# Optimization experiments

Measured on AMD Instinct MI355X. Metric: run time of the kernel, lower is better.

The kernel has to match this reference:

```python
import jax, jax.numpy as jnp
import numpy as np

B, L, NE, DOUT = 4, 4096, 64, 64
DI = 128          # backbone model dim (hardcoded d_inner in MambaDoc)
NL = 2            # num_layers
H = 2             # num_heads
N = 128           # state_dim
G = 1             # num_groups
CONV = 4          # conv_size
DIN = 2 * DI      # expand=2 -> 256 inner channels of the mixer
P = DIN // H      # headdim = 128
CCH = DIN + 2 * G * N      # 512 conv channels (x, B, C)
DPROJ = 2 * DIN + 2 * G * N + H  # 770 in_proj output width


def setup_inputs() -> dict:
    key = jax.random.key(0)
    ks = jax.random.split(key, 8)
    s = lambda k, shape, sc: (jax.random.normal(k, shape, jnp.float32) * sc)
    return {
        "x": s(ks[0], (B, L, NE), 1.0),
        "in_w": s(ks[1], (DI, NE), (1.0 / NE) ** 0.5),
        "in_b": jnp.zeros((DI,), jnp.float32),
        "out_w": s(ks[2], (DOUT, DI), (1.0 / DI) ** 0.5),
        "out_b": jnp.zeros((DOUT,), jnp.float32),
        "l_rms_w": jnp.ones((NL, DI), jnp.float32),
        "l_in_w": s(ks[3], (NL, DPROJ, DI), (1.0 / DI) ** 0.5),
        "conv_w": s(ks[4], (NL, CCH, CONV), (1.0 / CONV) ** 0.5),
        "conv_b": jnp.zeros((NL, CCH), jnp.float32),
        "dt_bias": s(ks[5], (NL, H), 0.1),
        "A_log": jnp.zeros((NL, H), jnp.float32),   # A = -exp(A_log) = -1
        "D_p": jnp.ones((NL, H), jnp.float32),
        "gnorm_w": jnp.ones((NL, DIN), jnp.float32),
        "l_out_w": s(ks[6], (NL, DI, DIN), (1.0 / DIN) ** 0.5),
        "fnorm_w": jnp.ones((DI,), jnp.float32),
    }


def _rms(x, w, eps=1e-5):
    return x * jax.lax.rsqrt(jnp.mean(x * x, -1, keepdims=True) + eps) * w


def _mamba_layer(x, rms_w, in_w, cw, cb, dtb, a_log, d, gnw, ow):
    # x: (B,L,DI)
    h = _rms(x, rms_w)
    zxbcdt = jnp.einsum("bld,ed->ble", h, in_w)  # (B,L,770)
    z, xBC, dt = jnp.split(zxbcdt, [DIN, DIN + CCH], axis=-1)
    # causal depthwise conv over time, conv_size taps
    xp = jnp.pad(xBC, ((0, 0), (CONV - 1, 0), (0, 0)))
    xc = cb + sum(xp[:, k:k + L, :] * cw[:, k] for k in range(CONV))
    xc = jax.nn.silu(xc)
    xs, Bm, Cm = jnp.split(xc, [DIN, DIN + G * N], axis=-1)
    xs = xs.reshape(B, L, H, P)
    dt = jax.nn.softplus(dt + dtb)                 # (B,L,H)
    dA = jnp.exp(dt * (-jnp.exp(a_log)))           # (B,L,H) discrete decay

    def step(hc, inp):
        dA_t, dt_t, x_t, B_t, C_t = inp  # (B,H),(B,H),(B,H,P),(B,N),(B,N)
        hc = hc * dA_t[:, :, None, None] + (dt_t[:, :, None] * x_t)[..., None] * B_t[:, None, None, :]
        y = jnp.einsum("bhpn,bn->bhp", hc, C_t)
        return hc, y

    h0 = jnp.zeros((B, H, P, N), x.dtype)
    seq = (jnp.moveaxis(dA, 1, 0), jnp.moveaxis(dt, 1, 0), jnp.moveaxis(xs, 1, 0),
           jnp.moveaxis(Bm, 1, 0), jnp.moveaxis(Cm, 1, 0))
    _, ys = jax.lax.scan(step, h0, seq)
    y = jnp.moveaxis(ys, 0, 1)                     # (B,L,H,P)
    y = y + xs * d[None, None, :, None]            # D skip connection
    y = _rms(y.reshape(B, L, DIN) * jax.nn.silu(z), gnw)  # gated RMSNorm
    return x + jnp.einsum("ble,de->bld", y, ow)


def reference(x, in_w, in_b, out_w, out_b, l_rms_w, l_in_w, conv_w, conv_b,
              dt_bias, A_log, D_p, gnorm_w, l_out_w, fnorm_w):
    xp = jnp.einsum("bln,dn->bld", x, in_w) + in_b
    h = xp
    for i in range(NL):
        h = _mamba_layer(h, l_rms_w[i], l_in_w[i], conv_w[i], conv_b[i],
                         dt_bias[i], A_log[i], D_p[i], gnorm_w[i], l_out_w[i])
    h = _rms(h, fnorm_w)            # backbone final norm
    out = xp + h                    # outer residual in MambaDoc.forward
    return jnp.einsum("bld,od->blo", out, out_w) + out_b
```

## Files before the change

kernel.cpp:

```cpp
#include <hip/hip_runtime.h>
#include <cstddef>
#include <cstdint>


#define LSEQ 4096
#define MTOK 16384

typedef unsigned short u16;
typedef _Float16 f16x8 __attribute__((ext_vector_type(8)));
typedef float f32x4 __attribute__((ext_vector_type(4)));

__device__ __forceinline__ u16 f2h(float x) {
    return __builtin_bit_cast(u16, (_Float16)x);
}
__device__ __forceinline__ float h2f(u16 u) {
    return (float)__builtin_bit_cast(_Float16, u);
}
__device__ __forceinline__ float silu_f(float x) { return x / (1.f + __expf(-x)); }

__device__ __forceinline__ void async_lds16(const void* g, void* l) {
    __builtin_amdgcn_global_load_lds(
        (const __attribute__((address_space(1))) unsigned int*)g,
        (__attribute__((address_space(3))) unsigned int*)l, 16, 0, 0);
}

__device__ __forceinline__ uint4 cvt8(const float* __restrict__ src) {
    float4 a = *(const float4*)src;
    float4 b = *(const float4*)(src + 4);
    union { u16 u[8]; uint4 q; } pk;
    pk.u[0] = f2h(a.x); pk.u[1] = f2h(a.y); pk.u[2] = f2h(a.z); pk.u[3] = f2h(a.w);
    pk.u[4] = f2h(b.x); pk.u[5] = f2h(b.y); pk.u[6] = f2h(b.z); pk.u[7] = f2h(b.w);
    return pk.q;
}

__device__ __forceinline__ uint4 cvt8g(const float* __restrict__ src,
                                       const float* __restrict__ gw) {
    float4 a = *(const float4*)src;
    float4 b = *(const float4*)(src + 4);
    float4 ga = *(const float4*)gw;
    float4 gb = *(const float4*)(gw + 4);
    union { u16 u[8]; uint4 q; } pk;
    pk.u[0] = f2h(a.x * ga.x); pk.u[1] = f2h(a.y * ga.y);
    pk.u[2] = f2h(a.z * ga.z); pk.u[3] = f2h(a.w * ga.w);
    pk.u[4] = f2h(b.x * gb.x); pk.u[5] = f2h(b.y * gb.y);
    pk.u[6] = f2h(b.z * gb.z); pk.u[7] = f2h(b.w * gb.w);
    return pk.q;
}

__global__ __launch_bounds__(256) void gemm_rms0_kernel(
    const float* __restrict__ xf, const float* __restrict__ wf,
    const float* __restrict__ bias, const float* __restrict__ rmsw,
    u16* __restrict__ xp16, u16* __restrict__ hbuf16, u16* __restrict__ hn16)
{
    __shared__ u16 sA[64 * 64];
    __shared__ u16 sW[128 * 64];
    __shared__ float red[64][33];
    __shared__ float srstd[64];
    const int m0 = blockIdx.y * 64;
    const int tid = threadIdx.x, wid = tid >> 6, lane = tid & 63;
    const int wm = (wid >> 1) * 32, wn = (wid & 1) * 64;
    const int quad = lane >> 4, cl = lane & 15;
    #pragma unroll
    for (int i = 0; i < 2; i++) {
        int ck = i * 256 + tid;
        int r = ck >> 3, cc = ck & 7;
        int csw = (cc ^ (r & 7)) << 3;
        *(uint4*)&sA[ck * 8] = cvt8(xf + (size_t)(m0 + r) * 64 + csw);
    }
    #pragma unroll
    for (int i = 0; i < 4; i++) {
        int ck = i * 256 + tid;
        int r = ck >> 3, cc = ck & 7;
        int csw = (cc ^ (r & 7)) << 3;
        *(uint4*)&sW[ck * 8] = cvt8(wf + (size_t)r * 64 + csw);
    }
    __syncthreads();
    f32x4 acc[2][4];
    #pragma unroll
    for (int i = 0; i < 2; i++)
        #pragma unroll
        for (int j = 0; j < 4; j++) acc[i][j] = f32x4{0.f, 0.f, 0.f, 0.f};
    #pragma unroll
    for (int ks = 0; ks < 2; ks++) {
        f16x8 af[2], wv[4];
        int kc = ks * 4 + quad;
        #pragma unroll
        for (int i = 0; i < 2; i++) {
            int r = wm + i * 16 + cl;
            af[i] = *(const f16x8*)&sA[r * 64 + ((kc ^ (r & 7)) << 3)];
        }
        #pragma unroll
        for (int j = 0; j < 4; j++) {
            int r = wn + j * 16 + cl;
            wv[j] = *(const f16x8*)&sW[r * 64 + ((kc ^ (r & 7)) << 3)];
        }
        #pragma unroll
        for (int i = 0; i < 2; i++)
            #pragma unroll
            for (int j = 0; j < 4; j++)
                acc[i][j] = __builtin_amdgcn_mfma_f32_16x16x32_f16(
                    af[i], wv[j], acc[i][j], 0, 0, 0);
    }
    const int slot = (wid & 1) * 16 + cl;
    #pragma unroll
    for (int i = 0; i < 2; i++)
        #pragma unroll
        for (int r = 0; r < 4; r++) {
            int t = wm + i * 16 + quad * 4 + r;
            float ssp = 0.f;
            #pragma unroll
            for (int j = 0; j < 4; j++) {
                int n = wn + j * 16 + cl;
                float v = acc[i][j][r] + bias[n];
                acc[i][j][r] = v;
                ssp += v * v;
            }
            red[t][slot] = ssp;
        }
    __syncthreads();
    if (tid < 64) {
        float s = 0.f;
        #pragma unroll
        for (int sl = 0; sl < 32; sl++) s += red[tid][sl];
        srstd[tid] = rsqrtf(s * (1.f / 128.f) + 1e-5f);
    }
    __syncthreads();
    #pragma unroll
    for (int i = 0; i < 2; i++)
        #pragma unroll
        for (int r = 0; r < 4; r++) {
            int t = wm + i * 16 + quad * 4 + r;
            size_t ob = (size_t)(m0 + t) * 128;
            float rstd = srstd[t];
            #pragma unroll
            for (int j = 0; j < 4; j++) {
                int n = wn + j * 16 + cl;
                float v = acc[i][j][r];
                u16 vh = f2h(v);
                xp16[ob + n] = vh;
                hbuf16[ob + n] = vh;
                hn16[ob + n] = f2h(v * rstd * rmsw[n]);
            }
        }
}

__global__ __launch_bounds__(256) void gemm_inproj_kernel(
    const u16* __restrict__ A, const float* __restrict__ Wf,
    u16* __restrict__ zx16, float* __restrict__ dtb, float* __restrict__ Sb,
    const float* __restrict__ dt_bias, const float* __restrict__ A_log)
{
    __shared__ u16 sA[128 * 64];
    __shared__ u16 sW[128 * 64];
    __shared__ float sdt[2][128];
    const int K = 128, N = 770;
    const int n0 = blockIdx.x * 128, m0 = blockIdx.y * 128;
    const int tid = threadIdx.x, wid = tid >> 6, lane = tid & 63;
    const int wm = (wid >> 1) * 64, wn = (wid & 1) * 64;
    const int quad = lane >> 4, cl = lane & 15;
    f32x4 acc[4][4];
    #pragma unroll
    for (int i = 0; i < 4; i++)
        #pragma unroll
        for (int j = 0; j < 4; j++) acc[i][j] = f32x4{0.f, 0.f, 0.f, 0.f};

    for (int k0 = 0; k0 < K; k0 += 64) {
        #pragma unroll
        for (int i = 0; i < 4; i++) {
            int ck = i * 256 + tid;
            int r = ck >> 3, cc = ck & 7;
            int csw = (cc ^ (r & 7)) << 3;
            async_lds16(A + (size_t)(m0 + r) * K + k0 + csw,
                        (void*)(sA + (i * 256 + (tid & ~63)) * 8));
        }
        #pragma unroll
        for (int i = 0; i < 4; i++) {
            int ck = i * 256 + tid;
            int r = ck >> 3, cc = ck & 7;
            int csw = (cc ^ (r & 7)) << 3;
            int rr = n0 + r; if (rr >= N) rr = N - 1;
            *(uint4*)&sW[ck * 8] = cvt8(Wf + (size_t)rr * K + k0 + csw);
        }
        __syncthreads();
        #pragma unroll
        for (int ks = 0; ks < 2; ks++) {
            f16x8 af[4], wv[4];
            int kc = ks * 4 + quad;
            #pragma unroll
            for (int i = 0; i < 4; i++) {
                int r = wm + i * 16 + cl;
                af[i] = *(const f16x8*)&sA[r * 64 + ((kc ^ (r & 7)) << 3)];
            }
            #pragma unroll
            for (int j = 0; j < 4; j++) {
                int r = wn + j * 16 + cl;
                wv[j] = *(const f16x8*)&sW[r * 64 + ((kc ^ (r & 7)) << 3)];
            }
            #pragma unroll
            for (int i = 0; i < 4; i++)
                #pragma unroll
                for (int j = 0; j < 4; j++)
                    acc[i][j] = __builtin_amdgcn_mfma_f32_16x16x32_f16(
                        af[i], wv[j], acc[i][j], 0, 0, 0);
        }
        __syncthreads();
    }
    if (blockIdx.x < 6) {
        #pragma unroll
        for (int i = 0; i < 4; i++) {
            int m = m0 + wm + i * 16 + quad * 4;
            #pragma unroll
            for (int j = 0; j < 4; j++) {
                int n = n0 + wn + j * 16 + cl;
                #pragma unroll
                for (int r = 0; r < 4; r++)
                    zx16[(size_t)(m + r) * 768 + n] = f2h(acc[i][j][r]);
            }
        }
    } else {
        if ((wid & 1) == 0 && cl < 2) {
            #pragma unroll
            for (int i = 0; i < 4; i++)
                #pragma unroll
                for (int r = 0; r < 4; r++)
                    sdt[cl][wm + i * 16 + quad * 4 + r] = acc[i][0][r];
        }
        __syncthreads();
        const int hh = tid >> 7, t = tid & 127;
        float raw = sdt[hh][t] + dt_bias[hh];
        float dt = fmaxf(raw, 0.f) + log1pf(__expf(-fabsf(raw)));
        dtb[(size_t)(m0 + t) * 2 + hh] = dt;
        float ad = -__expf(A_log[hh]) * dt;
        __syncthreads();
        sdt[hh][t] = ad;
        __syncthreads();
        for (int off = 1; off < 128; off <<= 1) {
            float add = (t >= off) ? sdt[hh][t - off] : 0.f;
            __syncthreads();
            sdt[hh][t] += add;
            __syncthreads();
        }
        Sb[(size_t)(m0 + t) * 2 + hh] = sdt[hh][t];
    }
}

__global__ __launch_bounds__(512) void chunkstate_conv_kernel(
    const u16* __restrict__ zx16, const float* __restrict__ cw,
    const float* __restrict__ cb, const float* __restrict__ dtb,
    const float* __restrict__ Sb, u16* __restrict__ Hb)
{
    __shared__ u16 XT[128 * 128];
    __shared__ u16 BT[128 * 128];
    __shared__ float scw[2][128][4];
    __shared__ float scb[2][128];
    __shared__ float ssw[128];
    const int c = blockIdx.x, h = blockIdx.y, b = blockIdx.z;
    const int tid = threadIdx.x, wid = tid >> 6, lane = tid & 63;
    const int quad = lane >> 4, cl = lane & 15;
    const int tok0 = b * LSEQ + c * 128;
    for (int idx = tid; idx < 256; idx += 512) {
        int grp = idx >> 7, j = idx & 127;
        int ch = grp ? (256 + j) : (128 * h + j);
        float4 w4 = *(const float4*)&cw[ch * 4];
        scw[grp][j][0] = w4.x; scw[grp][j][1] = w4.y;
        scw[grp][j][2] = w4.z; scw[grp][j][3] = w4.w;
        scb[grp][j] = cb[ch];
    }
    if (tid < 128) {
        float Sl = Sb[(size_t)(tok0 + 127) * 2 + h];
        ssw[tid] = __expf(Sl - Sb[(size_t)(tok0 + tid) * 2 + h])
                   * dtb[(size_t)(tok0 + tid) * 2 + h];
    }
    const int pg = tid >> 5, sb = tid & 31, s0 = sb * 4;
    const u16* gx = zx16 + 256 + 128 * h + pg * 8;
    const u16* gb = zx16 + 512 + pg * 8;
    uint4 vX[7], vB[7];
    #pragma unroll
    for (int i = 0; i < 7; i++) {
        int q = s0 - 3 + i;
        bool zer = (c == 0) && (q < 0);
        int qq = zer ? 0 : q;
        size_t off = (size_t)(tok0 + qq) * 768;
        uint4 xv = *(const uint4*)(gx + off);
        uint4 bv = *(const uint4*)(gb + off);
        vX[i] = zer ? make_uint4(0u, 0u, 0u, 0u) : xv;
        vB[i] = zer ? make_uint4(0u, 0u, 0u, 0u) : bv;
    }
    __syncthreads();
    #pragma unroll
    for (int j = 0; j < 4; j++) {
        int s = s0 + j;
        f16x8 a0 = __builtin_bit_cast(f16x8, vX[j]);
        f16x8 a1 = __builtin_bit_cast(f16x8, vX[j + 1]);
        f16x8 a2 = __builtin_bit_cast(f16x8, vX[j + 2]);
        f16x8 a3 = __builtin_bit_cast(f16x8, vX[j + 3]);
        #pragma unroll
        for (int jj = 0; jj < 8; jj++) {
            int p = pg * 8 + jj;
            float o = scb[0][p] + (float)a0[jj] * scw[0][p][0]
                    + (float)a1[jj] * scw[0][p][1]
                    + (float)a2[jj] * scw[0][p][2]
                    + (float)a3[jj] * scw[0][p][3];
            XT[p * 128 + (((s >> 3) ^ (p & 15)) << 3) + (s & 7)] = f2h(silu_f(o));
        }
    }
    #pragma unroll
    for (int j = 0; j < 4; j++) {
        int s = s0 + j;
        float wsv = ssw[s];
        f16x8 a0 = __builtin_bit_cast(f16x8, vB[j]);
        f16x8 a1 = __builtin_bit_cast(f16x8, vB[j + 1]);
        f16x8 a2 = __builtin_bit_cast(f16x8, vB[j + 2]);
        f16x8 a3 = __builtin_bit_cast(f16x8, vB[j + 3]);
        #pragma unroll
        for (int jj = 0; jj < 8; jj++) {
            int n = pg * 8 + jj;
            float o = scb[1][n] + (float)a0[jj] * scw[1][n][0]
                    + (float)a1[jj] * scw[1][n][1]
                    + (float)a2[jj] * scw[1][n][2]
                    + (float)a3[jj] * scw[1][n][3];
            o = silu_f(o) * wsv;
            BT[n * 128 + (((s >> 3) ^ (n & 15)) << 3) + (s & 7)] = f2h(o);
        }
    }
    __syncthreads();
    const size_t blk = ((size_t)((b * 2 + h) * 32 + c)) << 14;
    const int wm = (wid >> 1) * 32, wn = (wid & 1) * 64;
    f32x4 acc[2][4];
    #pragma unroll
    for (int i = 0; i < 2; i++)
        #pragma unroll
        for (int j = 0; j < 4; j++) acc[i][j] = f32x4{0.f, 0.f, 0.f, 0.f};
    #pragma unroll
    for (int ks = 0; ks < 4; ks++) {
        f16x8 xa[2], bb[4];
        int kc = ks * 4 + quad;
        #pragma unroll
        for (int i = 0; i < 2; i++) {
            int r = wm + i * 16 + cl;
            xa[i] = *(const f16x8*)&XT[r * 128 + ((kc ^ (r & 15)) << 3)];
        }
        #pragma unroll
        for (int j = 0; j < 4; j++) {
            int r = wn + j * 16 + cl;
            bb[j] = *(const f16x8*)&BT[r * 128 + ((kc ^ (r & 15)) << 3)];
        }
        #pragma unroll
        for (int i = 0; i < 2; i++)
            #pragma unroll
            for (int j = 0; j < 4; j++)
                acc[i][j] = __builtin_amdgcn_mfma_f32_16x16x32_f16(
                    xa[i], bb[j], acc[i][j], 0, 0, 0);
    }
    u16* out = Hb + blk;
    #pragma unroll
    for (int i = 0; i < 2; i++)
        #pragma unroll
        for (int j = 0; j < 4; j++)
            #pragma unroll
            for (int r = 0; r < 4; r++)
                out[(size_t)(wm + i * 16 + quad * 4 + r) * 128 + wn + j * 16 + cl]
                    = f2h(acc[i][j][r]);
}

__global__ __launch_bounds__(256) void statecombine_kernel(
    const float* __restrict__ Sb, const u16* __restrict__ Hb,
    u16* __restrict__ Hbf)
{
    __shared__ float sdec[32];
    const int h = blockIdx.y, b = blockIdx.z;
    const int e2 = blockIdx.x * 256 + threadIdx.x;
    if (threadIdx.x < 32)
        sdec[threadIdx.x] =
            __expf(Sb[(size_t)(b * LSEQ + threadIdx.x * 128 + 127) * 2 + h]);
    const size_t base2 = ((size_t)((b * 2 + h) * 32)) << 13;
    const unsigned int* src = (const unsigned int*)Hb;
    unsigned int* dst = (unsigned int*)Hbf;
    unsigned int v[32];
    #pragma unroll
    for (int c = 0; c < 32; c++)
        v[c] = src[base2 + ((size_t)c << 13) + e2];
    __syncthreads();
    float s0 = 0.f, s1 = 0.f;
    #pragma unroll
    for (int c = 0; c < 32; c++) {
        union { u16 u[2]; unsigned int q; } pk;
        pk.u[0] = f2h(s0); pk.u[1] = f2h(s1);
        dst[base2 + ((size_t)c << 13) + e2] = pk.q;
        float d = sdec[c];
        s0 = d * s0 + h2f((u16)(v[c] & 0xffffu));
        s1 = d * s1 + h2f((u16)(v[c] >> 16));
    }
}

__global__ __launch_bounds__(512) void ssd_ph_kernel(
    const u16* __restrict__ zx16, const u16* __restrict__ Hbf,
    const float* __restrict__ dtb, const float* __restrict__ Sb,
    const float* __restrict__ cw, const float* __restrict__ cb,
    const float* __restrict__ Dp, u16* __restrict__ g16)
{
    __shared__ u16 raw[128 * 128];
    __shared__ u16 XT[128 * 128];
    __shared__ u16 Btok[128 * 128];
    __shared__ u16 Ctok[128 * 128];
    __shared__ float sS[128], sdt[128];
    __shared__ float scw[3][128][4];
    __shared__ float scb[3][128];
    const int c = blockIdx.x, h = blockIdx.y, b = blockIdx.z;
    const int tid = threadIdx.x, wid = tid >> 6, lane = tid & 63;
    const int quad = lane >> 4, cl = lane & 15;
    const int tok0 = b * LSEQ + c * 128;
    const size_t blk = ((size_t)((b * 2 + h) * 32 + c)) << 14;
    for (int idx = tid; idx < 384; idx += 512) {
        int grp = idx >> 7, j = idx & 127;
        int ch = (grp == 0) ? (128 * h + j) : (grp == 1 ? 256 + j : 384 + j);
        float4 w4 = *(const float4*)&cw[ch * 4];
        scw[grp][j][0] = w4.x; scw[grp][j][1] = w4.y;
        scw[grp][j][2] = w4.z; scw[grp][j][3] = w4.w;
        scb[grp][j] = cb[ch];
    }
    if (tid < 128) {
        sS[tid] = Sb[(size_t)(tok0 + tid) * 2 + h];
        sdt[tid] = dtb[(size_t)(tok0 + tid) * 2 + h];
    }
    #pragma unroll
    for (int i = 0; i < 4; i++) {
        int ck = i * 512 + tid;
        int r = ck >> 4, cc = ck & 15;
        async_lds16(Hbf + blk + (size_t)r * 128 + ((cc ^ (r & 15)) << 3),
                    (void*)(raw + (i * 512 + (tid & ~63)) * 8));
    }
    const int pg = tid >> 5, sb = tid & 31, s0 = sb * 4;
    const u16* gx = zx16 + 256 + 128 * h + pg * 8;
    const u16* gb = zx16 + 512 + pg * 8;
    const u16* gc = zx16 + 640 + pg * 8;
    uint4 vX[7], vB[7], vC[7];
    #pragma unroll
    for (int i = 0; i < 7; i++) {
        int q = s0 - 3 + i;
        bool zer = (c == 0) && (q < 0);
        int qq = zer ? 0 : q;
        size_t off = (size_t)(tok0 + qq) * 768;
        uint4 xv = *(const uint4*)(gx + off);
        uint4 bv = *(const uint4*)(gb + off);
        uint4 cv = *(const uint4*)(gc + off);
        vX[i] = zer ? make_uint4(0u, 0u, 0u, 0u) : xv;
        vB[i] = zer ? make_uint4(0u, 0u, 0u, 0u) : bv;
        vC[i] = zer ? make_uint4(0u, 0u, 0u, 0u) : cv;
    }
    __syncthreads();
    #pragma unroll
    for (int j = 0; j < 4; j++) {
        int s = s0 + j;
        f16x8 a0 = __builtin_bit_cast(f16x8, vX[j]);
        f16x8 a1 = __builtin_bit_cast(f16x8, vX[j + 1]);
        f16x8 a2 = __builtin_bit_cast(f16x8, vX[j + 2]);
        f16x8 a3 = __builtin_bit_cast(f16x8, vX[j + 3]);
        #pragma unroll
        for (int jj = 0; jj < 8; jj++) {
            int p = pg * 8 + jj;
            float o = scb[0][p] + (float)a0[jj] * scw[0][p][0]
                    + (float)a1[jj] * scw[0][p][1]
                    + (float)a2[jj] * scw[0][p][2]
                    + (float)a3[jj] * scw[0][p][3];
            XT[p * 128 + (((s >> 3) ^ (p & 15)) << 3) + (s & 7)] = f2h(silu_f(o));
        }
    }
    #pragma unroll
    for (int j = 0; j < 4; j++) {
        int t = s0 + j;
        f16x8 a0 = __builtin_bit_cast(f16x8, vB[j]);
        f16x8 a1 = __builtin_bit_cast(f16x8, vB[j + 1]);
        f16x8 a2 = __builtin_bit_cast(f16x8, vB[j + 2]);
        f16x8 a3 = __builtin_bit_cast(f16x8, vB[j + 3]);
        union { u16 u[8]; uint4 q; } pk;
        #pragma unroll
        for (int jj = 0; jj < 8; jj++) {
            int n = pg * 8 + jj;
            float o = scb[1][n] + (float)a0[jj] * scw[1][n][0]
                    + (float)a1[jj] * scw[1][n][1]
                    + (float)a2[jj] * scw[1][n][2]
                    + (float)a3[jj] * scw[1][n][3];
            pk.u[jj] = f2h(silu_f(o));
        }
        *(uint4*)&Btok[t * 128 + ((pg ^ (t & 15)) << 3)] = pk.q;
    }
    #pragma unroll
    for (int j = 0; j < 4; j++) {
        int t = s0 + j;
        f16x8 a0 = __builtin_bit_cast(f16x8, vC[j]);
        f16x8 a1 = __builtin_bit_cast(f16x8, vC[j + 1]);
        f16x8 a2 = __builtin_bit_cast(f16x8, vC[j + 2]);
        f16x8 a3 = __builtin_bit_cast(f16x8, vC[j + 3]);
        union { u16 u[8]; uint4 q; } pk;
        #pragma unroll
        for (int jj = 0; jj < 8; jj++) {
            int n = pg * 8 + jj;
            float o = scb[2][n] + (float)a0[jj] * scw[2][n][0]
                    + (float)a1[jj] * scw[2][n][1]
                    + (float)a2[jj] * scw[2][n][2]
                    + (float)a3[jj] * scw[2][n][3];
            pk.u[jj] = f2h(silu_f(o));
        }
        *(uint4*)&Ctok[t * 128 + ((pg ^ (t & 15)) << 3)] = pk.q;
    }
    __syncthreads();
    const int wm = (wid >> 1) * 32, wn = (wid & 1) * 64;
    f32x4 acc[2][4];
    #pragma unroll
    for (int i = 0; i < 2; i++)
        #pragma unroll
        for (int j = 0; j < 4; j++) acc[i][j] = f32x4{0.f, 0.f, 0.f, 0.f};
    #pragma unroll
    for (int ks = 0; ks < 4; ks++) {
        f16x8 ca[2], hb[4];
        int kc = ks * 4 + quad;
        #pragma unroll
        for (int i = 0; i < 2; i++) {
            int r = wm + i * 16 + cl;
            ca[i] = *(const f16x8*)&Ctok[r * 128 + ((kc ^ (r & 15)) << 3)];
        }
        #pragma unroll
        for (int j = 0; j < 4; j++) {
            int r = wn + j * 16 + cl;
            hb[j] = *(const f16x8*)&raw[r * 128 + ((kc ^ (r & 15)) << 3)];
        }
        #pragma unroll
        for (int i = 0; i < 2; i++)
            #pragma unroll
            for (int j = 0; j < 4; j++)
                acc[i][j] = __builtin_amdgcn_mfma_f32_16x16x32_f16(
                    ca[i], hb[j], acc[i][j], 0, 0, 0);
    }
    #pragma unroll
    for (int i = 0; i < 2; i++)
        #pragma unroll
        for (int r = 0; r < 4; r++) {
            float e = __expf(sS[wm + i * 16 + quad * 4 + r]);
            #pragma unroll
            for (int j = 0; j < 4; j++) acc[i][j][r] *= e;
        }
    f32x4 sacc[2][4];
    #pragma unroll
    for (int i = 0; i < 2; i++)
        #pragma unroll
        for (int j = 0; j < 4; j++) sacc[i][j] = f32x4{0.f, 0.f, 0.f, 0.f};
    #pragma unroll
    for (int ks = 0; ks < 4; ks++) {
        f16x8 cs[2], bs[4];
        int kc = ks * 4 + quad;
        #pragma unroll
        for (int i2 = 0; i2 < 2; i2++) {
            int r = wm + i2 * 16 + cl;
            cs[i2] = *(const f16x8*)&Ctok[r * 128 + ((kc ^ (r & 15)) << 3)];
        }
        #pragma unroll
        for (int j = 0; j < 4; j++) {
            int r = wn + j * 16 + cl;
            bs[j] = *(const f16x8*)&Btok[r * 128 + ((kc ^ (r & 15)) << 3)];
        }
        #pragma unroll
        for (int i2 = 0; i2 < 2; i2++)
            #pragma unroll
            for (int j = 0; j < 4; j++)
                if (wm + i2 * 16 + 15 >= wn + j * 16)
                    sacc[i2][j] = __builtin_amdgcn_mfma_f32_16x16x32_f16(
                        cs[i2], bs[j], sacc[i2][j], 0, 0, 0);
    }
    __syncthreads();
    #pragma unroll
    for (int i2 = 0; i2 < 2; i2++)
        #pragma unroll
        for (int r = 0; r < 4; r++) {
            int t = wm + i2 * 16 + quad * 4 + r;
            float Stv = sS[t];
            #pragma unroll
            for (int j = 0; j < 4; j++) {
                int s = wn + j * 16 + cl;
                float gv = 0.f;
                if (s <= t) gv = sacc[i2][j][r] * __expf(Stv - sS[s]) * sdt[s];
                raw[t * 128 + (((s >> 3) ^ (t & 15)) << 3) + (s & 7)] = f2h(gv);
            }
        }
    __syncthreads();
    #pragma unroll
    for (int ks = 0; ks < 4; ks++) {
        f16x8 ga[2], xb[4];
        int kc = ks * 4 + quad;
        #pragma unroll
        for (int i = 0; i < 2; i++) {
            int r = wm + i * 16 + cl;
            ga[i] = *(const f16x8*)&raw[r * 128 + ((kc ^ (r & 15)) << 3)];
        }
        #pragma unroll
        for (int j = 0; j < 4; j++) {
            int r = wn + j * 16 + cl;
            xb[j] = *(const f16x8*)&XT[r * 128 + ((kc ^ (r & 15)) << 3)];
        }
        #pragma unroll
        for (int i = 0; i < 2; i++)
            #pragma unroll
            for (int j = 0; j < 4; j++)
                acc[i][j] = __builtin_amdgcn_mfma_f32_16x16x32_f16(
                    ga[i], xb[j], acc[i][j], 0, 0, 0);
    }
    const float dco = Dp[h];
    #pragma unroll
    for (int i = 0; i < 2; i++)
        #pragma unroll
        for (int r = 0; r < 4; r++) {
            int t = wm + i * 16 + quad * 4 + r;
            u16* row = g16 + (size_t)(tok0 + t) * 256 + h * 128;
            #pragma unroll
            for (int j = 0; j < 4; j++) {
                int p = wn + j * 16 + cl;
                float xv = h2f(XT[p * 128 + (((t >> 3) ^ (p & 15)) << 3) + (t & 7)]);
                float zv = h2f(zx16[(size_t)(tok0 + t) * 768 + h * 128 + p]);
                row[p] = f2h((acc[i][j][r] + dco * xv) * silu_f(zv));
            }
        }
}

__global__ __launch_bounds__(256) void gemm_outrms_kernel(
    const u16* __restrict__ A, const float* __restrict__ Wf,
    const float* __restrict__ gnw, const float* __restrict__ rmsw,
    u16* __restrict__ xp16, u16* __restrict__ hbuf16, u16* __restrict__ hn16,
    const float* __restrict__ out_wf, const float* __restrict__ out_b,
    float* __restrict__ dout, int mode)
{
    __shared__ u16 sA[64 * 64];
    __shared__ u16 sW[128 * 64];
    __shared__ float red[64][33];
    __shared__ float srstd[64];
    __shared__ float redp[64][5];
    __shared__ float rstdg[64];
    __shared__ u16 hn2[64 * 128];
    __shared__ u16 ow[64 * 128];
    const int K = 256;
    const int m0 = blockIdx.y * 64;
    const int tid = threadIdx.x, wid = tid >> 6, lane = tid & 63;
    const int wm = (wid >> 1) * 32, wn = (wid & 1) * 64;
    const int quad = lane >> 4, cl = lane & 15;
    f32x4 acc[2][4];
    #pragma unroll
    for (int i = 0; i < 2; i++)
        #pragma unroll
        for (int j = 0; j < 4; j++) acc[i][j] = f32x4{0.f, 0.f, 0.f, 0.f};

    float ssq = 0.f;
    for (int k0 = 0; k0 < K; k0 += 64) {
        #pragma unroll
        for (int i = 0; i < 2; i++) {
            int ck = i * 256 + tid;
            int r = ck >> 3, cc = ck & 7;
            int csw = (cc ^ (r & 7)) << 3;
            async_lds16(A + (size_t)(m0 + r) * K + k0 + csw,
                        (void*)(sA + (i * 256 + (tid & ~63)) * 8));
        }
        #pragma unroll
        for (int i = 0; i < 4; i++) {
            int ck = i * 256 + tid;
            int r = ck >> 3, cc = ck & 7;
            int csw = (cc ^ (r & 7)) << 3;
            *(uint4*)&sW[ck * 8] = cvt8g(Wf + (size_t)r * K + k0 + csw,
                                         gnw + k0 + csw);
        }
        __syncthreads();
        {
            int rr = tid >> 2, q = tid & 3;
            f16x8 v0 = *(const f16x8*)&sA[rr * 64 + q * 16];
            f16x8 v1 = *(const f16x8*)&sA[rr * 64 + q * 16 + 8];
            #pragma unroll
            for (int j = 0; j < 8; j++) {
                float a = (float)v0[j], bq = (float)v1[j];
                ssq += a * a + bq * bq;
            }
        }
        #pragma unroll
        for (int ks = 0; ks < 2; ks++) {
            f16x8 af[2], wv[4];
            int kc = ks * 4 + quad;
            #pragma unroll
            for (int i = 0; i < 2; i++) {
                int r = wm + i * 16 + cl;
                af[i] = *(const f16x8*)&sA[r * 64 + ((kc ^ (r & 7)) << 3)];
            }
            #pragma unroll
            for (int j = 0; j < 4; j++) {
                int r = wn + j * 16 + cl;
                wv[j] = *(const f16x8*)&sW[r * 64 + ((kc ^ (r & 7)) << 3)];
            }
            #pragma unroll
            for (int i = 0; i < 2; i++)
                #pragma unroll
                for (int j = 0; j < 4; j++)
                    acc[i][j] = __builtin_amdgcn_mfma_f32_16x16x32_f16(
                        af[i], wv[j], acc[i][j], 0, 0, 0);
        }
        __syncthreads();
    }
    redp[tid >> 2][tid & 3] = ssq;
    __syncthreads();
    if (tid < 64)
        rstdg[tid] = rsqrtf((redp[tid][0] + redp[tid][1] + redp[tid][2]
                             + redp[tid][3]) * (1.f / 256.f) + 1e-5f);
    __syncthreads();
    const int slot = (wid & 1) * 16 + cl;
    #pragma unroll
    for (int i = 0; i < 2; i++)
        #pragma unroll
        for (int r = 0; r < 4; r++) {
            int t = wm + i * 16 + quad * 4 + r;
            size_t ob = (size_t)(m0 + t) * 128;
            float rg = rstdg[t];
            float ssp = 0.f;
            #pragma unroll
            for (int j = 0; j < 4; j++) {
                int n = wn + j * 16 + cl;
                float v = acc[i][j][r] * rg + h2f(hbuf16[ob + n]);
                acc[i][j][r] = v;
                ssp += v * v;
            }
            red[t][slot] = ssp;
        }
    __syncthreads();
    if (tid < 64) {
        float s = 0.f;
        #pragma unroll
        for (int sl = 0; sl < 32; sl++) s += red[tid][sl];
        srstd[tid] = rsqrtf(s * (1.f / 128.f) + 1e-5f);
    }
    __syncthreads();
    #pragma unroll
    for (int i = 0; i < 2; i++)
        #pragma unroll
        for (int r = 0; r < 4; r++) {
            int t = wm + i * 16 + quad * 4 + r;
            size_t ob = (size_t)(m0 + t) * 128;
            float rstd = srstd[t];
            #pragma unroll
            for (int j = 0; j < 4; j++) {
                int n = wn + j * 16 + cl;
                float v = acc[i][j][r];
                float val = v * rstd * rmsw[n];
                if (mode == 1) {
                    hbuf16[ob + n] = f2h(v);
                    hn16[ob + n] = f2h(val);
                } else {
                    val += h2f(xp16[ob + n]);
                    hn2[t * 128 + (((n >> 3) ^ (t & 15)) << 3) + (n & 7)] = f2h(val);
                }
            }
        }
    if (mode == 1) return;
    #pragma unroll
    for (int i = 0; i < 4; i++) {
        int ck = i * 256 + tid;
        int rr = ck >> 4, cc = ck & 15;
        int csw = (cc ^ (rr & 15)) << 3;
        *(uint4*)&ow[ck * 8] = cvt8(out_wf + (size_t)rr * 128 + csw);
    }
    __syncthreads();
    const int wm4 = (wid >> 1) * 32, wn4 = (wid & 1) * 32;
    f32x4 acc2[2][2];
    #pragma unroll
    for (int i = 0; i < 2; i++)
        #pragma unroll
        for (int j = 0; j < 2; j++) acc2[i][j] = f32x4{0.f, 0.f, 0.f, 0.f};
    #pragma unroll
    for (int ks = 0; ks < 4; ks++) {
        f16x8 af2[2], wf2[2];
        int kc = ks * 4 + quad;
        #pragma unroll
        for (int i = 0; i < 2; i++) {
            int r = wm4 + i * 16 + cl;
            af2[i] = *(const f16x8*)&hn2[r * 128 + ((kc ^ (r & 15)) << 3)];
        }
        #pragma unroll
        for (int j = 0; j < 2; j++) {
            int rr = wn4 + j * 16 + cl;
            wf2[j] = *(const f16x8*)&ow[rr * 128 + ((kc ^ (rr & 15)) << 3)];
        }
        #pragma unroll
        for (int i = 0; i < 2; i++)
            #pragma unroll
            for (int j = 0; j < 2; j++)
                acc2[i][j] = __builtin_amdgcn_mfma_f32_16x16x32_f16(
                    af2[i], wf2[j], acc2[i][j], 0, 0, 0);
    }
    #pragma unroll
    for (int i = 0; i < 2; i++) {
        int m = m0 + wm4 + i * 16 + quad * 4;
        #pragma unroll
        for (int j = 0; j < 2; j++) {
            int n = wn4 + j * 16 + cl;
            float bv = out_b[n];
            #pragma unroll
            for (int r = 0; r < 4; r++)
                dout[(size_t)(m + r) * 64 + n] = acc2[i][j][r] + bv;
        }
    }
}

extern "C" void kernel_launch(void* const* d_in, const int* in_sizes, int n_in,
                              void* d_out, int out_size, void* d_ws, size_t ws_size,
                              hipStream_t stream)
{
    (void)in_sizes; (void)n_in; (void)out_size; (void)ws_size;
    const float* x       = (const float*)d_in[0];
    const float* in_w    = (const float*)d_in[1];
    const float* in_b    = (const float*)d_in[2];
    const float* out_w   = (const float*)d_in[3];
    const float* out_b   = (const float*)d_in[4];
    const float* l_rms_w = (const float*)d_in[5];
    const float* l_in_w  = (const float*)d_in[6];
    const float* conv_w  = (const float*)d_in[7];
    const float* conv_b  = (const float*)d_in[8];
    const float* dt_bias = (const float*)d_in[9];
    const float* A_log   = (const float*)d_in[10];
    const float* D_p     = (const float*)d_in[11];
    const float* gnorm_w = (const float*)d_in[12];
    const float* l_out_w = (const float*)d_in[13];
    const float* fnorm_w = (const float*)d_in[14];

    char* w = (char*)d_ws;
    u16*   xp16   = (u16*)(w);
    u16*   hbuf16 = (u16*)(w + 4194304);
    u16*   hn16   = (u16*)(w + 8388608);
    u16*   zx16   = (u16*)(w + 12582912);
    float* dtb    = (float*)(w + 37748736);
    float* Sb     = (float*)(w + 37879808);
    u16*   Hb     = (u16*)(w + 38010880);
    u16*   Hbf    = (u16*)(w + 46399488);
    u16*   g16    = (u16*)(w + 54788096);

    gemm_rms0_kernel<<<dim3(1, 256), 256, 0, stream>>>(
        x, in_w, in_b, l_rms_w, xp16, hbuf16, hn16);

    for (int i = 0; i < 2; i++) {
        gemm_inproj_kernel<<<dim3(7, 128), 256, 0, stream>>>(
            hn16, l_in_w + (size_t)i * 770 * 128, zx16, dtb, Sb,
            dt_bias + i * 2, A_log + i * 2);
        chunkstate_conv_kernel<<<dim3(32, 2, 4), 512, 0, stream>>>(
            zx16, conv_w + i * 2048, conv_b + i * 512, dtb, Sb, Hb);
        statecombine_kernel<<<dim3(32, 2, 4), 256, 0, stream>>>(Sb, Hb, Hbf);
        ssd_ph_kernel<<<dim3(32, 2, 4), 512, 0, stream>>>(
            zx16, Hbf, dtb, Sb, conv_w + i * 2048, conv_b + i * 512,
            D_p + i * 2, g16);
        gemm_outrms_kernel<<<dim3(1, 256), 256, 0, stream>>>(
            g16, l_out_w + (size_t)i * 128 * 256, gnorm_w + i * 256,
            (i == 0) ? (l_rms_w + 128) : fnorm_w, xp16, hbuf16, hn16,
            out_w, out_b, (float*)d_out, (i == 0) ? 1 : 3);
    }
}
```

Measured before the change: 229.6 us.

## Fuse chunk-state, state-combine and SSD kernels into one cooperative grid-synced kernel

Merges the chunk-state/conv, inter-chunk state combine, and per-chunk SSD output kernels into a single cooperative kernel that uses grid-wide syncs between phases. The conv and silu of x/B/C is now computed once instead of twice, and two launches are removed. The chunk-state prefix states are now read directly from global memory instead of being staged in LDS asynchronously. The change adds two grid barriers, and the cooperative launch requires all 256 blocks of 512 threads to be co-resident, which the heavier LDS use could make harder.

```diff
diff --git a/kernel.cpp b/kernel.cpp
--- a/kernel.cpp
+++ b/kernel.cpp
@@ -1,10 +1,12 @@
 #include <hip/hip_runtime.h>
+#include <hip/hip_cooperative_groups.h>
 #include <cstddef>
 #include <cstdint>
 
+namespace cg = cooperative_groups;
+
 
 #define LSEQ 4096
-#define MTOK 16384
 
 typedef unsigned short u16;
 typedef _Float16 f16x8 __attribute__((ext_vector_type(8)));
@@ -243,173 +245,28 @@
     }
 }
 
-__global__ __launch_bounds__(512) void chunkstate_conv_kernel(
+__global__ __launch_bounds__(512) void fused_mamba_kernel(
     const u16* __restrict__ zx16, const float* __restrict__ cw,
     const float* __restrict__ cb, const float* __restrict__ dtb,
-    const float* __restrict__ Sb, u16* __restrict__ Hb)
+    const float* __restrict__ Sb, u16* __restrict__ Hb,
+    u16* __restrict__ Hbf, const float* __restrict__ Dp,
+    u16* __restrict__ g16)
 {
     __shared__ u16 XT[128 * 128];
-    __shared__ u16 BT[128 * 128];
-    __shared__ float scw[2][128][4];
-    __shared__ float scb[2][128];
-    __shared__ float ssw[128];
-    const int c = blockIdx.x, h = blockIdx.y, b = blockIdx.z;
-    const int tid = threadIdx.x, wid = tid >> 6, lane = tid & 63;
-    const int quad = lane >> 4, cl = lane & 15;
-    const int tok0 = b * LSEQ + c * 128;
-    for (int idx = tid; idx < 256; idx += 512) {
-        int grp = idx >> 7, j = idx & 127;
-        int ch = grp ? (256 + j) : (128 * h + j);
-        float4 w4 = *(const float4*)&cw[ch * 4];
-        scw[grp][j][0] = w4.x; scw[grp][j][1] = w4.y;
-        scw[grp][j][2] = w4.z; scw[grp][j][3] = w4.w;
-        scb[grp][j] = cb[ch];
-    }
-    if (tid < 128) {
-        float Sl = Sb[(size_t)(tok0 + 127) * 2 + h];
-        ssw[tid] = __expf(Sl - Sb[(size_t)(tok0 + tid) * 2 + h])
-                   * dtb[(size_t)(tok0 + tid) * 2 + h];
-    }
-    const int pg = tid >> 5, sb = tid & 31, s0 = sb * 4;
-    const u16* gx = zx16 + 256 + 128 * h + pg * 8;
-    const u16* gb = zx16 + 512 + pg * 8;
-    uint4 vX[7], vB[7];
-    #pragma unroll
-    for (int i = 0; i < 7; i++) {
-        int q = s0 - 3 + i;
-        bool zer = (c == 0) && (q < 0);
-        int qq = zer ? 0 : q;
-        size_t off = (size_t)(tok0 + qq) * 768;
-        uint4 xv = *(const uint4*)(gx + off);
-        uint4 bv = *(const uint4*)(gb + off);
-        vX[i] = zer ? make_uint4(0u, 0u, 0u, 0u) : xv;
-        vB[i] = zer ? make_uint4(0u, 0u, 0u, 0u) : bv;
-    }
-    __syncthreads();
-    #pragma unroll
-    for (int j = 0; j < 4; j++) {
-        int s = s0 + j;
-        f16x8 a0 = __builtin_bit_cast(f16x8, vX[j]);
-        f16x8 a1 = __builtin_bit_cast(f16x8, vX[j + 1]);
-        f16x8 a2 = __builtin_bit_cast(f16x8, vX[j + 2]);
-        f16x8 a3 = __builtin_bit_cast(f16x8, vX[j + 3]);
-        #pragma unroll
-        for (int jj = 0; jj < 8; jj++) {
-            int p = pg * 8 + jj;
-            float o = scb[0][p] + (float)a0[jj] * scw[0][p][0]
-                    + (float)a1[jj] * scw[0][p][1]
-                    + (float)a2[jj] * scw[0][p][2]
-                    + (float)a3[jj] * scw[0][p][3];
-            XT[p * 128 + (((s >> 3) ^ (p & 15)) << 3) + (s & 7)] = f2h(silu_f(o));
-        }
-    }
-    #pragma unroll
-    for (int j = 0; j < 4; j++) {
-        int s = s0 + j;
-        float wsv = ssw[s];
-        f16x8 a0 = __builtin_bit_cast(f16x8, vB[j]);
-        f16x8 a1 = __builtin_bit_cast(f16x8, vB[j + 1]);
-        f16x8 a2 = __builtin_bit_cast(f16x8, vB[j + 2]);
-        f16x8 a3 = __builtin_bit_cast(f16x8, vB[j + 3]);
-        #pragma unroll
-        for (int jj = 0; jj < 8; jj++) {
-            int n = pg * 8 + jj;
-            float o = scb[1][n] + (float)a0[jj] * scw[1][n][0]
-                    + (float)a1[jj] * scw[1][n][1]
-                    + (float)a2[jj] * scw[1][n][2]
-                    + (float)a3[jj] * scw[1][n][3];
-            o = silu_f(o) * wsv;
-            BT[n * 128 + (((s >> 3) ^ (n & 15)) << 3) + (s & 7)] = f2h(o);
-        }
-    }
-    __syncthreads();
-    const size_t blk = ((size_t)((b * 2 + h) * 32 + c)) << 14;
-    const int wm = (wid >> 1) * 32, wn = (wid & 1) * 64;
-    f32x4 acc[2][4];
-    #pragma unroll
-    for (int i = 0; i < 2; i++)
-        #pragma unroll
-        for (int j = 0; j < 4; j++) acc[i][j] = f32x4{0.f, 0.f, 0.f, 0.f};
-    #pragma unroll
-    for (int ks = 0; ks < 4; ks++) {
-        f16x8 xa[2], bb[4];
-        int kc = ks * 4 + quad;
-        #pragma unroll
-        for (int i = 0; i < 2; i++) {
-            int r = wm + i * 16 + cl;
-            xa[i] = *(const f16x8*)&XT[r * 128 + ((kc ^ (r & 15)) << 3)];
-        }
-        #pragma unroll
-        for (int j = 0; j < 4; j++) {
-            int r = wn + j * 16 + cl;
-            bb[j] = *(const f16x8*)&BT[r * 128 + ((kc ^ (r & 15)) << 3)];
-        }
-        #pragma unroll
-        for (int i = 0; i < 2; i++)
-            #pragma unroll
-            for (int j = 0; j < 4; j++)
-                acc[i][j] = __builtin_amdgcn_mfma_f32_16x16x32_f16(
-                    xa[i], bb[j], acc[i][j], 0, 0, 0);
-    }
-    u16* out = Hb + blk;
-    #pragma unroll
-    for (int i = 0; i < 2; i++)
-        #pragma unroll
-        for (int j = 0; j < 4; j++)
-            #pragma unroll
-            for (int r = 0; r < 4; r++)
-                out[(size_t)(wm + i * 16 + quad * 4 + r) * 128 + wn + j * 16 + cl]
-                    = f2h(acc[i][j][r]);
-}
-
-__global__ __launch_bounds__(256) void statecombine_kernel(
-    const float* __restrict__ Sb, const u16* __restrict__ Hb,
-    u16* __restrict__ Hbf)
-{
-    __shared__ float sdec[32];
-    const int h = blockIdx.y, b = blockIdx.z;
-    const int e2 = blockIdx.x * 256 + threadIdx.x;
-    if (threadIdx.x < 32)
-        sdec[threadIdx.x] =
-            __expf(Sb[(size_t)(b * LSEQ + threadIdx.x * 128 + 127) * 2 + h]);
-    const size_t base2 = ((size_t)((b * 2 + h) * 32)) << 13;
-    const unsigned int* src = (const unsigned int*)Hb;
-    unsigned int* dst = (unsigned int*)Hbf;
-    unsigned int v[32];
-    #pragma unroll
-    for (int c = 0; c < 32; c++)
-        v[c] = src[base2 + ((size_t)c << 13) + e2];
-    __syncthreads();
-    float s0 = 0.f, s1 = 0.f;
-    #pragma unroll
-    for (int c = 0; c < 32; c++) {
-        union { u16 u[2]; unsigned int q; } pk;
-        pk.u[0] = f2h(s0); pk.u[1] = f2h(s1);
-        dst[base2 + ((size_t)c << 13) + e2] = pk.q;
-        float d = sdec[c];
-        s0 = d * s0 + h2f((u16)(v[c] & 0xffffu));
-        s1 = d * s1 + h2f((u16)(v[c] >> 16));
-    }
-}
-
-__global__ __launch_bounds__(512) void ssd_ph_kernel(
-    const u16* __restrict__ zx16, const u16* __restrict__ Hbf,
-    const float* __restrict__ dtb, const float* __restrict__ Sb,
-    const float* __restrict__ cw, const float* __restrict__ cb,
-    const float* __restrict__ Dp, u16* __restrict__ g16)
-{
-    __shared__ u16 raw[128 * 128];
-    __shared__ u16 XT[128 * 128];
+    __shared__ u16 BTw[128 * 128];
     __shared__ u16 Btok[128 * 128];
     __shared__ u16 Ctok[128 * 128];
-    __shared__ float sS[128], sdt[128];
+    __shared__ float sS[128], sdt[128], ssw[128];
     __shared__ float scw[3][128][4];
     __shared__ float scb[3][128];
+    __shared__ float sdec[32];
     const int c = blockIdx.x, h = blockIdx.y, b = blockIdx.z;
     const int tid = threadIdx.x, wid = tid >> 6, lane = tid & 63;
     const int quad = lane >> 4, cl = lane & 15;
     const int tok0 = b * LSEQ + c * 128;
     const size_t blk = ((size_t)((b * 2 + h) * 32 + c)) << 14;
+    const int wm = (wid >> 1) * 32, wn = (wid & 1) * 64;
+
     for (int idx = tid; idx < 384; idx += 512) {
         int grp = idx >> 7, j = idx & 127;
         int ch = (grp == 0) ? (128 * h + j) : (grp == 1 ? 256 + j : 384 + j);
@@ -419,15 +276,12 @@
         scb[grp][j] = cb[ch];
     }
     if (tid < 128) {
-        sS[tid] = Sb[(size_t)(tok0 + tid) * 2 + h];
-        sdt[tid] = dtb[(size_t)(tok0 + tid) * 2 + h];
-    }
-    #pragma unroll
-    for (int i = 0; i < 4; i++) {
-        int ck = i * 512 + tid;
-        int r = ck >> 4, cc = ck & 15;
-        async_lds16(Hbf + blk + (size_t)r * 128 + ((cc ^ (r & 15)) << 3),
-                    (void*)(raw + (i * 512 + (tid & ~63)) * 8));
+        float Sv = Sb[(size_t)(tok0 + tid) * 2 + h];
+        float dtv = dtb[(size_t)(tok0 + tid) * 2 + h];
+        float Sl = Sb[(size_t)(tok0 + 127) * 2 + h];
+        sS[tid] = Sv;
+        sdt[tid] = dtv;
+        ssw[tid] = __expf(Sl - Sv) * dtv;
     }
     const int pg = tid >> 5, sb = tid & 31, s0 = sb * 4;
     const u16* gx = zx16 + 256 + 128 * h + pg * 8;
@@ -468,6 +322,7 @@
     #pragma unroll
     for (int j = 0; j < 4; j++) {
         int t = s0 + j;
+        float wsv = ssw[t];
         f16x8 a0 = __builtin_bit_cast(f16x8, vB[j]);
         f16x8 a1 = __builtin_bit_cast(f16x8, vB[j + 1]);
         f16x8 a2 = __builtin_bit_cast(f16x8, vB[j + 2]);
@@ -480,7 +335,9 @@
                     + (float)a1[jj] * scw[1][n][1]
                     + (float)a2[jj] * scw[1][n][2]
                     + (float)a3[jj] * scw[1][n][3];
-            pk.u[jj] = f2h(silu_f(o));
+            float so = silu_f(o);
+            pk.u[jj] = f2h(so);
+            BTw[n * 128 + (((t >> 3) ^ (n & 15)) << 3) + (t & 7)] = f2h(so * wsv);
         }
         *(uint4*)&Btok[t * 128 + ((pg ^ (t & 15)) << 3)] = pk.q;
     }
@@ -504,32 +361,96 @@
         *(uint4*)&Ctok[t * 128 + ((pg ^ (t & 15)) << 3)] = pk.q;
     }
     __syncthreads();
-    const int wm = (wid >> 1) * 32, wn = (wid & 1) * 64;
+    {
+        f32x4 hacc[2][4];
+        #pragma unroll
+        for (int i = 0; i < 2; i++)
+            #pragma unroll
+            for (int j = 0; j < 4; j++) hacc[i][j] = f32x4{0.f, 0.f, 0.f, 0.f};
+        #pragma unroll
+        for (int ks = 0; ks < 4; ks++) {
+            f16x8 xa[2], bb[4];
+            int kc = ks * 4 + quad;
+            #pragma unroll
+            for (int i = 0; i < 2; i++) {
+                int r = wm + i * 16 + cl;
+                xa[i] = *(const f16x8*)&XT[r * 128 + ((kc ^ (r & 15)) << 3)];
+            }
+            #pragma unroll
+            for (int j = 0; j < 4; j++) {
+                int r = wn + j * 16 + cl;
+                bb[j] = *(const f16x8*)&BTw[r * 128 + ((kc ^ (r & 15)) << 3)];
+            }
+            #pragma unroll
+            for (int i = 0; i < 2; i++)
+                #pragma unroll
+                for (int j = 0; j < 4; j++)
+                    hacc[i][j] = __builtin_amdgcn_mfma_f32_16x16x32_f16(
+                        xa[i], bb[j], hacc[i][j], 0, 0, 0);
+        }
+        u16* out = Hb + blk;
+        #pragma unroll
+        for (int i = 0; i < 2; i++)
+            #pragma unroll
+            for (int j = 0; j < 4; j++)
+                #pragma unroll
+                for (int r = 0; r < 4; r++)
+                    out[(size_t)(wm + i * 16 + quad * 4 + r) * 128
+                        + wn + j * 16 + cl] = f2h(hacc[i][j][r]);
+    }
+    cg::this_grid().sync();
+    if (tid < 32)
+        sdec[tid] = __expf(Sb[(size_t)(b * LSEQ + tid * 128 + 127) * 2 + h]);
+    __syncthreads();
+    if (tid < 256) {
+        const int e2 = c * 256 + tid;
+        const size_t base2 = ((size_t)((b * 2 + h) * 32)) << 13;
+        const unsigned int* src = (const unsigned int*)Hb;
+        unsigned int* dst = (unsigned int*)Hbf;
+        unsigned int v[32];
+        #pragma unroll
+        for (int c2 = 0; c2 < 32; c2++)
+            v[c2] = src[base2 + ((size_t)c2 << 13) + e2];
+        float s0f = 0.f, s1f = 0.f;
+        #pragma unroll
+        for (int c2 = 0; c2 < 32; c2++) {
+            union { u16 u[2]; unsigned int q; } pk;
+            pk.u[0] = f2h(s0f); pk.u[1] = f2h(s1f);
+            dst[base2 + ((size_t)c2 << 13) + e2] = pk.q;
+            float d = sdec[c2];
+            s0f = d * s0f + h2f((u16)(v[c2] & 0xffffu));
+            s1f = d * s1f + h2f((u16)(v[c2] >> 16));
+        }
+    }
+    cg::this_grid().sync();
     f32x4 acc[2][4];
     #pragma unroll
     for (int i = 0; i < 2; i++)
         #pragma unroll
         for (int j = 0; j < 4; j++) acc[i][j] = f32x4{0.f, 0.f, 0.f, 0.f};
-    #pragma unroll
-    for (int ks = 0; ks < 4; ks++) {
-        f16x8 ca[2], hb[4];
-        int kc = ks * 4 + quad;
-        #pragma unroll
-        for (int i = 0; i < 2; i++) {
-            int r = wm + i * 16 + cl;
-            ca[i] = *(const f16x8*)&Ctok[r * 128 + ((kc ^ (r & 15)) << 3)];
-        }
-        #pragma unroll
-        for (int j = 0; j < 4; j++) {
-            int r = wn + j * 16 + cl;
-            hb[j] = *(const f16x8*)&raw[r * 128 + ((kc ^ (r & 15)) << 3)];
-        }
-        #pragma unroll
-        for (int i = 0; i < 2; i++)
-            #pragma unroll
-            for (int j = 0; j < 4; j++)
-                acc[i][j] = __builtin_amdgcn_mfma_f32_16x16x32_f16(
-                    ca[i], hb[j], acc[i][j], 0, 0, 0);
+    {
+        const u16* hg = Hbf + blk;
+        #pragma unroll
+        for (int ks = 0; ks < 4; ks++) {
+            f16x8 ca[2], hb[4];
+            int kc = ks * 4 + quad;
+            #pragma unroll
+            for (int i = 0; i < 2; i++) {
+                int r = wm + i * 16 + cl;
+                ca[i] = *(const f16x8*)&Ctok[r * 128 + ((kc ^ (r & 15)) << 3)];
+            }
+            #pragma unroll
+            for (int j = 0; j < 4; j++) {
+                int r = wn + j * 16 + cl;
+                hb[j] = *(const f16x8*)(hg + (size_t)r * 128 + kc * 8);
+            }
+            #pragma unroll
+            for (int i = 0; i < 2; i++)
+                #pragma unroll
+                for (int j = 0; j < 4; j++)
+                    acc[i][j] = __builtin_amdgcn_mfma_f32_16x16x32_f16(
+                        ca[i], hb[j], acc[i][j], 0, 0, 0);
+        }
     }
     #pragma unroll
     for (int i = 0; i < 2; i++)
@@ -566,7 +487,6 @@
                     sacc[i2][j] = __builtin_amdgcn_mfma_f32_16x16x32_f16(
                         cs[i2], bs[j], sacc[i2][j], 0, 0, 0);
     }
-    __syncthreads();
     #pragma unroll
     for (int i2 = 0; i2 < 2; i2++)
         #pragma unroll
@@ -578,7 +498,7 @@
                 int s = wn + j * 16 + cl;
                 float gv = 0.f;
                 if (s <= t) gv = sacc[i2][j][r] * __expf(Stv - sS[s]) * sdt[s];
-                raw[t * 128 + (((s >> 3) ^ (t & 15)) << 3) + (s & 7)] = f2h(gv);
+                BTw[t * 128 + (((s >> 3) ^ (t & 15)) << 3) + (s & 7)] = f2h(gv);
             }
         }
     __syncthreads();
@@ -589,7 +509,7 @@
         #pragma unroll
         for (int i = 0; i < 2; i++) {
             int r = wm + i * 16 + cl;
-            ga[i] = *(const f16x8*)&raw[r * 128 + ((kc ^ (r & 15)) << 3)];
+            ga[i] = *(const f16x8*)&BTw[r * 128 + ((kc ^ (r & 15)) << 3)];
         }
         #pragma unroll
         for (int j = 0; j < 4; j++) {
@@ -840,12 +760,23 @@
         gemm_inproj_kernel<<<dim3(7, 128), 256, 0, stream>>>(
             hn16, l_in_w + (size_t)i * 770 * 128, zx16, dtb, Sb,
             dt_bias + i * 2, A_log + i * 2);
-        chunkstate_conv_kernel<<<dim3(32, 2, 4), 512, 0, stream>>>(
-            zx16, conv_w + i * 2048, conv_b + i * 512, dtb, Sb, Hb);
-        statecombine_kernel<<<dim3(32, 2, 4), 256, 0, stream>>>(Sb, Hb, Hbf);
-        ssd_ph_kernel<<<dim3(32, 2, 4), 512, 0, stream>>>(
-            zx16, Hbf, dtb, Sb, conv_w + i * 2048, conv_b + i * 512,
-            D_p + i * 2, g16);
+        {
+            const u16* zxp = zx16;
+            const float* cwp = conv_w + i * 2048;
+            const float* cbp = conv_b + i * 512;
+            const float* dtbp = dtb;
+            const float* Sbp = Sb;
+            u16* Hbp = Hb;
+            u16* Hbfp = Hbf;
+            const float* Dpp = D_p + i * 2;
+            u16* g16p = g16;
+            void* fargs[9] = { (void*)&zxp, (void*)&cwp, (void*)&cbp,
+                               (void*)&dtbp, (void*)&Sbp, (void*)&Hbp,
+                               (void*)&Hbfp, (void*)&Dpp, (void*)&g16p };
+            hipLaunchCooperativeKernel((void*)fused_mamba_kernel,
+                                       dim3(32, 2, 4), dim3(512),
+                                       fargs, 0, stream);
+        }
         gemm_outrms_kernel<<<dim3(1, 256), 256, 0, stream>>>(
             g16, l_out_w + (size_t)i * 128 * 256, gnorm_w + i * 256,
             (i == 0) ? (l_rms_w + 128) : fnorm_w, xp16, hbuf16, hn16,
```

Measured after the change: 401.8 us. +75.0%, slower.
